# Optimization experiments

Hardware: AMD Instinct MI355X
Metric: run time of the kernel (lower is better)

## Reference

```python
import jax, jax.numpy as jnp
import numpy as np

BN_EPS = 1e-6
SOFTMAX_EPS = 1e-8
D = 64      # fingerprint_dim
BD = 12     # bond_dim
N_ATOM = 10000
N_EDGE = 40000


def _bn(x, gamma, beta, mean, var):
    # BatchNorm1d in inference mode (running stats)
    return (x - mean) / jnp.sqrt(var + BN_EPS) * gamma + beta


def setup_inputs() -> dict:
    key = jax.random.key(0)
    ks = jax.random.split(key, 16)
    inp = {
        "atom": jax.random.normal(ks[0], (N_ATOM, D), dtype=jnp.float32),
        "bond_index": jax.random.randint(ks[1], (N_EDGE, 2), 0, N_ATOM, dtype=jnp.int64),
        "bond": jax.random.normal(ks[2], (N_EDGE, BD), dtype=jnp.float32),
        # encoder: Linear(bond_dim, D*D) + BatchNorm1d(D*D)
        "enc_W": jax.random.normal(ks[3], (D * D, BD), dtype=jnp.float32) * (1.0 / np.sqrt(BD)),
        "enc_b": jnp.zeros((D * D,), dtype=jnp.float32),
        "enc_gamma": jnp.ones((D * D,), dtype=jnp.float32),
        "enc_beta": jnp.zeros((D * D,), dtype=jnp.float32),
        "enc_mean": jnp.zeros((D * D,), dtype=jnp.float32),
        "enc_var": jnp.ones((D * D,), dtype=jnp.float32),
        # align: Linear(2*D, 1)
        "align_W": jax.random.normal(ks[4], (1, 2 * D), dtype=jnp.float32) * (1.0 / np.sqrt(2 * D)),
        "align_b": jnp.zeros((1,), dtype=jnp.float32),
        # attend: Linear(D, D) + BatchNorm1d(D), no activation
        "att_W": jax.random.normal(ks[5], (D, D), dtype=jnp.float32) * (1.0 / np.sqrt(D)),
        "att_b": jnp.zeros((D,), dtype=jnp.float32),
        "att_gamma": jnp.ones((D,), dtype=jnp.float32),
        "att_beta": jnp.zeros((D,), dtype=jnp.float32),
        "att_mean": jnp.zeros((D,), dtype=jnp.float32),
        "att_var": jnp.ones((D,), dtype=jnp.float32),
        # GRUCell(D, D)
        "gru_W_ih": jax.random.normal(ks[6], (3 * D, D), dtype=jnp.float32) * (1.0 / np.sqrt(D)),
        "gru_W_hh": jax.random.normal(ks[7], (3 * D, D), dtype=jnp.float32) * (1.0 / np.sqrt(D)),
        "gru_b_ih": jnp.zeros((3 * D,), dtype=jnp.float32),
        "gru_b_hh": jnp.zeros((3 * D,), dtype=jnp.float32),
    }
    return inp


def reference(atom, bond_index, bond,
              enc_W, enc_b, enc_gamma, enc_beta, enc_mean, enc_var,
              align_W, align_b,
              att_W, att_b, att_gamma, att_beta, att_mean, att_var,
              gru_W_ih, gru_W_hh, gru_b_ih, gru_b_hh):
    num_atom, d = atom.shape
    tgt = bond_index[:, 0]  # target atom of each edge
    nbr = bond_index[:, 1]  # neighbor atom of each edge

    # encoder: relu(BN(linear(bond))) -> per-edge [d, d] bond matrix
    enc = jax.nn.relu(_bn(bond @ enc_W.T + enc_b, enc_gamma, enc_beta, enc_mean, enc_var))
    enc = enc.reshape(-1, d, d)  # [E, d, d]

    # gather neighbor atoms, per-edge matvec through bond matrix
    neighbor = jnp.einsum('ed,edf->ef', atom[nbr], enc)  # [E, d]

    # attention logits (dropout is identity in eval)
    feat = jnp.concatenate([atom[tgt], neighbor], axis=-1)  # [E, 2d]
    score = jax.nn.leaky_relu(feat @ align_W.T + align_b, negative_slope=0.01)  # [E, 1]

    # segment softmax over target atoms
    mx = jax.ops.segment_max(score, tgt, num_segments=num_atom)  # [N, 1]
    ex = jnp.exp(score - mx[tgt])
    denom = jax.ops.segment_sum(ex, tgt, num_segments=num_atom)[tgt] + SOFTMAX_EPS
    attn = ex / denom  # [E, 1]

    # attend: BN(linear(neighbor)) (no activation), weighted scatter-add
    attd = _bn(neighbor @ att_W.T + att_b, att_gamma, att_beta, att_mean, att_var)
    context = jax.ops.segment_sum(attn * attd, tgt, num_segments=num_atom)  # [N, d]
    context = jax.nn.elu(context)

    # GRUCell(context, atom)
    gi = context @ gru_W_ih.T + gru_b_ih  # [N, 3d]
    gh = atom @ gru_W_hh.T + gru_b_hh     # [N, 3d]
    i_r, i_z, i_n = jnp.split(gi, 3, axis=-1)
    h_r, h_z, h_n = jnp.split(gh, 3, axis=-1)
    r = jax.nn.sigmoid(i_r + h_r)
    z = jax.nn.sigmoid(i_z + h_z)
    n = jnp.tanh(i_n + r * h_n)
    return (1.0 - z) * n + z * atom
```

## Files before the change

### kernel.cpp

```cpp
#include <hip/hip_runtime.h>
#include <math.h>

#define NA 10000
#define NE 40000

typedef float f4 __attribute__((ext_vector_type(4)));
typedef float f16v __attribute__((ext_vector_type(16)));
typedef int   i4 __attribute__((ext_vector_type(4)));
typedef __bf16 bf16x8 __attribute__((ext_vector_type(8)));

union U8 { unsigned short us[8]; bf16x8 v; };

static __device__ __forceinline__ unsigned short bf_rne(float x){
  unsigned u = __float_as_uint(x);
  unsigned r = (u + 0x7fffu + ((u>>16)&1u)) >> 16;
  return (unsigned short)r;
}
static __device__ __forceinline__ float bf_to_f(unsigned short h){
  return __uint_as_float(((unsigned)h)<<16);
}

__global__ __launch_bounds__(256) void k_pre(
  const float* __restrict__ encW, const float* __restrict__ encB,
  const float* __restrict__ eg, const float* __restrict__ ebt,
  const float* __restrict__ e_mn, const float* __restrict__ e_vr,
  const float* __restrict__ attW, const float* __restrict__ attB,
  const float* __restrict__ agm, const float* __restrict__ abt,
  const float* __restrict__ amn, const float* __restrict__ avr,
  const float* __restrict__ wih, const float* __restrict__ whh,
  const int* __restrict__ bidx, const float* __restrict__ atom,
  const float* __restrict__ alW,
  unsigned short* __restrict__ Bh, unsigned short* __restrict__ Bl,
  unsigned short* __restrict__ aBh, unsigned short* __restrict__ aBl,
  float* __restrict__ attBf, float* __restrict__ wT,
  float* __restrict__ p, int* __restrict__ cnt)
{
  int tid = threadIdx.x;
  int gid = blockIdx.x*256 + tid;
  int gstride = gridDim.x*256;
  for (int i=gid; i<65536; i+=gstride){
    int j = i&7, ll = (i>>3)&63, t = i>>9;
    int d = t>>1, ft = t&1;
    int k = ((ll>>5)<<3)+j;
    int n = d*64 + ft*32 + (ll&31);
    float s = eg[n]*rsqrtf(e_vr[n]+1e-6f);
    unsigned short vh=0, vl=0;
    if (k<12){
      float wv = encW[n*12+k]*s;
      unsigned short hi = bf_rne(wv);
      vh = hi; vl = bf_rne(wv - bf_to_f(hi));
    } else if (k==12){
      float b = (encB[n]-e_mn[n])*s + ebt[n];
      unsigned short hi = bf_rne(b);
      vh = hi; vl = bf_rne(b - bf_to_f(hi));
    }
    Bh[i] = vh; Bl[i] = vl;
  }
  for (int i=gid; i<4096; i+=gstride){
    int j=i&7, l=(i>>3)&63, t=i>>9;
    int kk=t>>1, nt=t&1;
    int k = kk*16 + ((l>>5)<<3) + j;
    int n = nt*32 + (l&31);
    float s = agm[n]*rsqrtf(avr[n]+1e-6f);
    float wv = attW[n*64+k]*s;
    unsigned short hi = bf_rne(wv);
    aBh[i]=hi; aBl[i]=bf_rne(wv - bf_to_f(hi));
  }
  for (int f=gid; f<64; f+=gstride){
    float s = agm[f]*rsqrtf(avr[f]+1e-6f);
    attBf[f] = (attB[f]-amn[f])*s + abt[f];
  }
  for (int i=gid; i<24576; i+=gstride){
    int j=i&3, f=(i>>2)&63, idx2=i>>8;
    int g=idx2>>4, kg=idx2&15, k=kg*4+j;
    wT[i] = (g<3)? wih[(g*64+f)*64+k] : whh[((g-3)*64+f)*64+k];
  }
  {
    int wid = gid>>6;
    int l = tid&63;
    float wl = alW[l];
    for (int a=wid; a<NA; a+=(gstride>>6)){
      float v = wl*atom[(size_t)a*64+l];
      v += __shfl_xor(v,1);  v += __shfl_xor(v,2);
      v += __shfl_xor(v,4);  v += __shfl_xor(v,8);
      v += __shfl_xor(v,16); v += __shfl_xor(v,32);
      if (l==0) p[a]=v;
    }
  }
  for (int e=gid; e<NE; e+=gstride) atomicAdd(&cnt[bidx[e*2]],1);
}

__global__ __launch_bounds__(256) void k_scan(const int* __restrict__ cnt,
                                              int* __restrict__ rowstart,
                                              int* __restrict__ wofs)
{
  __shared__ int sPart[256];
  int t = threadIdx.x;
  int base = t*40;
  i4 buf[10];
  int sum = 0;
  if (base < NA){
    const i4* cp = (const i4*)(cnt + base);
    #pragma unroll
    for (int i=0;i<10;i++) buf[i] = cp[i];
    #pragma unroll
    for (int i=0;i<10;i++) sum += buf[i].x+buf[i].y+buf[i].z+buf[i].w;
  }
  sPart[t]=sum;
  __syncthreads();
  for (int off=1; off<256; off<<=1){
    int v = (t>=off)? sPart[t-off] : 0;
    __syncthreads();
    sPart[t]+=v;
    __syncthreads();
  }
  int run = sPart[t]-sum;
  if (base < NA){
    #pragma unroll
    for (int i=0;i<10;i++){
      i4 b=buf[i], o;
      o.x=run; run+=b.x; o.y=run; run+=b.y;
      o.z=run; run+=b.z; o.w=run; run+=b.w;
      ((i4*)(rowstart+base))[i]=o;
      ((i4*)(wofs+base))[i]=o;
    }
  }
  if (t==0) rowstart[NA]=NE;
}

__global__ __launch_bounds__(256) void k_scatter(const int* __restrict__ bidx,
                                                 int* __restrict__ wofs,
                                                 int* __restrict__ elist)
{
  int e = blockIdx.x*256 + threadIdx.x;
  if (e < NE){
    int tg = bidx[e*2];
    int pos = atomicAdd(&wofs[tg],1);
    elist[pos]=e;
  }
}

__global__ __launch_bounds__(256) void k_edge(
  const float* __restrict__ atom, const int* __restrict__ bidx, const float* __restrict__ bond,
  const unsigned short* __restrict__ Bh, const unsigned short* __restrict__ Bl,
  const int* __restrict__ elist, float* __restrict__ nbC)
{
  __shared__ float sA[2304];
  __shared__ float sP[4096];
  __shared__ int   sEl[32];
  __shared__ int   sNbr[32];

  int tid = threadIdx.x;
  int l = tid & 63;
  int w = tid >> 6;
  int g = l >> 5;
  int em = l & 31;
  int E0 = blockIdx.x * 32;

  if (tid < 32){
    int e = elist[E0+tid];
    sEl[tid] = e;
    sNbr[tid] = bidx[e*2+1];
  }
  __syncthreads();
  for (int i=tid; i<2048; i+=256){
    int le=i>>6, d=i&63;
    sA[d*36+le] = atom[(size_t)sNbr[le]*64 + d];
  }

  U8 A1, A2;
  {
    const f4* bp = (const f4*)(bond + (size_t)sEl[em]*12);
    f4 b0=bp[0], b1v=bp[1], b2v=bp[2];
    float bv[12] = {b0.x,b0.y,b0.z,b0.w,b1v.x,b1v.y,b1v.z,b1v.w,b2v.x,b2v.y,b2v.z,b2v.w};
    unsigned short hi[12], lo2[12];
    #pragma unroll
    for (int j=0;j<12;j++){ hi[j]=bf_rne(bv[j]); lo2[j]=bf_rne(bv[j]-bf_to_f(hi[j])); }
    #pragma unroll
    for (int j=0;j<8;j++){
      int k = g*8+j;
      A1.us[j] = (k<12)? hi[k] : (k==12? (unsigned short)0x3F80 : (unsigned short)0);
      A2.us[j] = (k<12)? lo2[k] : (unsigned short)0;
    }
  }
  __syncthreads();

  int ft = w & 1;
  int dbase = (w >> 1) * 32;

  f4 nacc[4];
  #pragma unroll
  for (int q=0;q<4;q++) nacc[q] = (f4){0.f,0.f,0.f,0.f};
  f16v cz;
  #pragma unroll
  for (int r=0;r<16;r++) cz[r] = 0.f;

  U8 cbh, cbl;
  cbh.v = *(const bf16x8*)(Bh + ((size_t)((dbase*2+ft)*64 + l))*8);
  cbl.v = *(const bf16x8*)(Bl + ((size_t)((dbase*2+ft)*64 + l))*8);

  #pragma unroll 2
  for (int dd=0; dd<32; dd++){
    int d = dbase + dd;
    int dn = (dd<31)? d+1 : d;
    U8 nbh, nbl;
    nbh.v = *(const bf16x8*)(Bh + ((size_t)((dn*2+ft)*64 + l))*8);
    nbl.v = *(const bf16x8*)(Bl + ((size_t)((dn*2+ft)*64 + l))*8);

    f4 ldA[4];
    #pragma unroll
    for (int q=0;q<4;q++) ldA[q] = *(const f4*)&sA[d*36 + 8*q + 4*g];

    f16v c;
    c = __builtin_amdgcn_mfma_f32_32x32x16_bf16(A1.v, cbh.v, cz, 0,0,0);
    c = __builtin_amdgcn_mfma_f32_32x32x16_bf16(A2.v, cbh.v, c, 0,0,0);
    c = __builtin_amdgcn_mfma_f32_32x32x16_bf16(A1.v, cbl.v, c, 0,0,0);
    #pragma unroll
    for (int r=0;r<16;r++){
      float ev = fmaxf(c[r], 0.f);
      nacc[r>>2][r&3] = fmaf(ldA[r>>2][r&3], ev, nacc[r>>2][r&3]);
    }
    cbh = nbh; cbl = nbl;
  }

  #pragma unroll
  for (int r=0;r<16;r++)
    sP[w*1024 + r*64 + l] = nacc[r>>2][r&3];
  __syncthreads();

  if (w < 2){
    #pragma unroll 4
    for (int r=0;r<16;r++){
      int idx = r*64 + l;
      float v = sP[w*1024 + idx] + sP[(w+2)*1024 + idx];
      int m = (r&3) + ((r>>2)<<3) + ((l>>5)<<2);
      int f = (w<<5) + (l&31);
      nbC[(size_t)(E0+m)*64 + f] = v;
    }
  }
}

__global__ __launch_bounds__(256) void k_zq(
  const float* __restrict__ nbC,
  const unsigned short* __restrict__ aBh, const unsigned short* __restrict__ aBl,
  const float* __restrict__ alW,
  float* __restrict__ zC, float* __restrict__ qv)
{
  __shared__ float sNb[64*68];
  int tid = threadIdx.x;
  int l = tid & 63;
  int w = tid >> 6;
  int g = l >> 5;
  int em = l & 31;
  int E0 = blockIdx.x * 64;

  for (int i=tid; i<4096; i+=256){
    int le=i>>6, f=i&63;
    sNb[le*68+f] = nbC[(size_t)(E0+le)*64 + f];
  }
  __syncthreads();

  {
    float alwn = alW[64+l];
    #pragma unroll 4
    for (int i=0;i<16;i++){
      int le = w*16 + i;
      float qq = sNb[le*68 + l] * alwn;
      qq += __shfl_xor(qq,1);  qq += __shfl_xor(qq,2);
      qq += __shfl_xor(qq,4);  qq += __shfl_xor(qq,8);
      qq += __shfl_xor(qq,16); qq += __shfl_xor(qq,32);
      if (l==0) qv[E0+le] = qq;
    }
  }

  {
    f16v c;
    #pragma unroll
    for (int r=0;r<16;r++) c[r] = 0.f;
    int mt2 = w>>1, nt = w&1;
    #pragma unroll
    for (int kk=0; kk<4; kk++){
      const float* src = &sNb[(mt2*32+em)*68 + kk*16 + g*8];
      f4 x0 = *(const f4*)src;
      f4 x1 = *(const f4*)(src+4);
      U8 Ah, Al;
      #pragma unroll
      for (int j=0;j<4;j++){
        unsigned short h0 = bf_rne(x0[j]);
        Ah.us[j] = h0; Al.us[j] = bf_rne(x0[j]-bf_to_f(h0));
        unsigned short h1 = bf_rne(x1[j]);
        Ah.us[4+j] = h1; Al.us[4+j] = bf_rne(x1[j]-bf_to_f(h1));
      }
      U8 bh, bl;
      bh.v = *(const bf16x8*)(aBh + ((size_t)((kk*2+nt)*64 + l))*8);
      bl.v = *(const bf16x8*)(aBl + ((size_t)((kk*2+nt)*64 + l))*8);
      c = __builtin_amdgcn_mfma_f32_32x32x16_bf16(Ah.v, bh.v, c, 0,0,0);
      c = __builtin_amdgcn_mfma_f32_32x32x16_bf16(Al.v, bh.v, c, 0,0,0);
      c = __builtin_amdgcn_mfma_f32_32x32x16_bf16(Ah.v, bl.v, c, 0,0,0);
    }
    #pragma unroll
    for (int r=0;r<16;r++){
      int row = (r&3) + ((r>>2)<<3) + ((l>>5)<<2);
      zC[(size_t)(E0 + mt2*32 + row)*64 + nt*32 + (l&31)] = c[r];
    }
  }
}

__global__ __launch_bounds__(256, 4) void k_gru(
  const float* __restrict__ atom, const float* __restrict__ zC,
  const int* __restrict__ rowstart, const float* __restrict__ p,
  const float* __restrict__ qv, const float* __restrict__ alB,
  const float* __restrict__ attBf, const float* __restrict__ wT,
  const float* __restrict__ bih, const float* __restrict__ bhh,
  float* __restrict__ out)
{
  __shared__ float sc[4][2][64];
  __shared__ float shh[4][2][64];
  int tid = threadIdx.x;
  int l = tid & 63;
  int w = tid >> 6;
  int base = blockIdx.x*8 + w*2;
  float bias = attBf[l];
  float ab = alB[0];

  #pragma unroll
  for (int aa=0; aa<2; aa++){
    int a = base + aa;
    float cf=0.f, hf=0.f;
    if (a < NA){
      hf = atom[(size_t)a*64 + l];
      int d0 = rowstart[a];
      int deg = rowstart[a+1] - d0;
      if (deg > 0){
        float pa = p[a] + ab;
        float mx = -1e30f;
        #pragma unroll 1
        for (int i=0;i<deg;i++){
          float s = pa + qv[d0+i];
          s = (s>0.f)? s : 0.01f*s;
          mx = fmaxf(mx, s);
        }
        float dn = 0.f, y = 0.f;
        #pragma unroll 1
        for (int i=0;i<deg;i++){
          float s = pa + qv[d0+i];
          s = (s>0.f)? s : 0.01f*s;
          float ex = __expf(s - mx);
          dn += ex;
          y = fmaf(ex, zC[(size_t)(d0+i)*64 + l], y);
        }
        cf = (y + dn*bias)/(dn + 1e-8f);
        cf = (cf>0.f)? cf : expm1f(cf);
      }
    }
    sc[w][aa][l] = cf; shh[w][aa][l] = hf;
  }
  __syncthreads();

  float acc[6][2];
  #pragma unroll
  for (int gg=0;gg<6;gg++){ acc[gg][0]=0.f; acc[gg][1]=0.f; }

  #pragma unroll 2
  for (int kg=0; kg<16; kg++){
    f4 wv[6];
    #pragma unroll
    for (int gg=0;gg<6;gg++) wv[gg] = *(const f4*)&wT[(size_t)((gg*16+kg)*64 + l)*4];
    #pragma unroll
    for (int aa=0;aa<2;aa++){
      f4 cv = *(const f4*)&sc[w][aa][kg*4];
      f4 hv = *(const f4*)&shh[w][aa][kg*4];
      #pragma unroll
      for (int j=0;j<4;j++){
        acc[0][aa] = fmaf(cv[j], wv[0][j], acc[0][aa]);
        acc[1][aa] = fmaf(cv[j], wv[1][j], acc[1][aa]);
        acc[2][aa] = fmaf(cv[j], wv[2][j], acc[2][aa]);
        acc[3][aa] = fmaf(hv[j], wv[3][j], acc[3][aa]);
        acc[4][aa] = fmaf(hv[j], wv[4][j], acc[4][aa]);
        acc[5][aa] = fmaf(hv[j], wv[5][j], acc[5][aa]);
      }
    }
  }

  float b0 = bih[l], b1 = bih[64+l], b2 = bih[128+l];
  float h0 = bhh[l], h1 = bhh[64+l], h2 = bhh[128+l];
  #pragma unroll
  for (int aa=0;aa<2;aa++){
    int a = base + aa;
    if (a < NA){
      float hf = shh[w][aa][l];
      float r = 1.f/(1.f + expf(-(acc[0][aa] + b0 + acc[3][aa] + h0)));
      float z = 1.f/(1.f + expf(-(acc[1][aa] + b1 + acc[4][aa] + h1)));
      float n = tanhf(acc[2][aa] + b2 + r*(acc[5][aa] + h2));
      out[(size_t)a*64 + l] = (1.f - z)*n + z*hf;
    }
  }
}

extern "C" void kernel_launch(void* const* d_in, const int* in_sizes, int n_in,
                              void* d_out, int out_size, void* d_ws, size_t ws_size,
                              hipStream_t stream) {
  const float* atom = (const float*)d_in[0];
  const int*   bidx = (const int*)  d_in[1];
  const float* bond = (const float*)d_in[2];
  const float* encW = (const float*)d_in[3];
  const float* encB = (const float*)d_in[4];
  const float* eg   = (const float*)d_in[5];
  const float* ebt  = (const float*)d_in[6];
  const float* e_mn = (const float*)d_in[7];
  const float* e_vr = (const float*)d_in[8];
  const float* alW  = (const float*)d_in[9];
  const float* alB  = (const float*)d_in[10];
  const float* atW  = (const float*)d_in[11];
  const float* atB  = (const float*)d_in[12];
  const float* agm  = (const float*)d_in[13];
  const float* abt  = (const float*)d_in[14];
  const float* amn  = (const float*)d_in[15];
  const float* avr  = (const float*)d_in[16];
  const float* wih  = (const float*)d_in[17];
  const float* whh  = (const float*)d_in[18];
  const float* bih  = (const float*)d_in[19];
  const float* bhh  = (const float*)d_in[20];

  float* ws = (float*)d_ws;
  unsigned short* Bh  = (unsigned short*)(ws + 0);
  unsigned short* Bl  = (unsigned short*)(ws + 32768);
  unsigned short* aBh = (unsigned short*)(ws + 65536);
  unsigned short* aBl = (unsigned short*)(ws + 67584);
  float* attBf   = ws + 69632;
  float* wT      = ws + 69696;
  float* p       = ws + 94272;
  int*   cnt     = (int*)(ws + 104288);
  int*   rowstart= (int*)(ws + 114304);
  int*   wofs    = (int*)(ws + 124320);
  int*   elist   = (int*)(ws + 134336);
  float* qv      = ws + 174336;
  float* nbC     = ws + 214336;
  float* outp    = (float*)d_out;

  hipMemsetAsync(cnt, 0, NA*sizeof(int), stream);
  k_pre<<<512, 256, 0, stream>>>(encW,encB,eg,ebt,e_mn,e_vr,
                                 atW,atB,agm,abt,amn,avr,
                                 wih,whh,bidx,atom,alW,
                                 Bh,Bl,aBh,aBl,attBf,wT,p,cnt);
  k_scan<<<1, 256, 0, stream>>>(cnt, rowstart, wofs);
  k_scatter<<<(NE+255)/256, 256, 0, stream>>>(bidx, wofs, elist);
  k_edge<<<1250, 256, 0, stream>>>(atom, bidx, bond, Bh, Bl, elist, nbC);
  k_zq<<<625, 256, 0, stream>>>(nbC, aBh, aBl, alW, nbC , qv);
  k_gru<<<1250, 256, 0, stream>>>(atom, nbC, rowstart, p, qv, alB,
                                  attBf, wT, bih, bhh, outp);
}
```

Before: 187.3 us.

## Fuse edge neighbor computation with attention projection kernel, 64 edges per block

Merges k_edge and k_zq into one kernel. Each block now handles 64 edges instead of 32, and the per-edge neighbor vectors stay in shared memory (reusing sA) instead of going out to global memory and being read back. This removes one kernel launch and a full write plus read of the E×64 intermediate. It also reuses each loaded bond-matrix fragment across two MFMA tiles. In exchange, per-thread registers and shared memory grow and the grid halves to 625 blocks, which may lower occupancy and parallelism.

```diff
diff --git a/kernel.cpp b/kernel.cpp
--- a/kernel.cpp
+++ b/kernel.cpp
@@ -143,34 +143,37 @@
 __global__ __launch_bounds__(256) void k_edge(
   const float* __restrict__ atom, const int* __restrict__ bidx, const float* __restrict__ bond,
   const unsigned short* __restrict__ Bh, const unsigned short* __restrict__ Bl,
-  const int* __restrict__ elist, float* __restrict__ nbC)
+  const unsigned short* __restrict__ aBh, const unsigned short* __restrict__ aBl,
+  const float* __restrict__ alW,
+  const int* __restrict__ elist, float* __restrict__ zC, float* __restrict__ qv)
 {
-  __shared__ float sA[2304];
+  __shared__ float sA[4352];
   __shared__ float sP[4096];
-  __shared__ int   sEl[32];
-  __shared__ int   sNbr[32];
+  __shared__ int   sEl[64];
+  __shared__ int   sNbr[64];
 
   int tid = threadIdx.x;
   int l = tid & 63;
   int w = tid >> 6;
   int g = l >> 5;
   int em = l & 31;
-  int E0 = blockIdx.x * 32;
-
-  if (tid < 32){
+  int E0 = blockIdx.x * 64;
+
+  if (tid < 64){
     int e = elist[E0+tid];
     sEl[tid] = e;
     sNbr[tid] = bidx[e*2+1];
   }
   __syncthreads();
-  for (int i=tid; i<2048; i+=256){
+  for (int i=tid; i<4096; i+=256){
     int le=i>>6, d=i&63;
-    sA[d*36+le] = atom[(size_t)sNbr[le]*64 + d];
-  }
-
-  U8 A1, A2;
-  {
-    const f4* bp = (const f4*)(bond + (size_t)sEl[em]*12);
+    sA[d*68+le] = atom[(size_t)sNbr[le]*64 + d];
+  }
+
+  U8 A1[2], A2[2];
+  #pragma unroll
+  for (int t=0;t<2;t++){
+    const f4* bp = (const f4*)(bond + (size_t)sEl[t*32+em]*12);
     f4 b0=bp[0], b1v=bp[1], b2v=bp[2];
     float bv[12] = {b0.x,b0.y,b0.z,b0.w,b1v.x,b1v.y,b1v.z,b1v.w,b2v.x,b2v.y,b2v.z,b2v.w};
     unsigned short hi[12], lo2[12];
@@ -179,8 +182,8 @@
     #pragma unroll
     for (int j=0;j<8;j++){
       int k = g*8+j;
-      A1.us[j] = (k<12)? hi[k] : (k==12? (unsigned short)0x3F80 : (unsigned short)0);
-      A2.us[j] = (k<12)? lo2[k] : (unsigned short)0;
+      A1[t].us[j] = (k<12)? hi[k] : (k==12? (unsigned short)0x3F80 : (unsigned short)0);
+      A2[t].us[j] = (k<12)? lo2[k] : (unsigned short)0;
     }
   }
   __syncthreads();
@@ -188,9 +191,11 @@
   int ft = w & 1;
   int dbase = (w >> 1) * 32;
 
-  f4 nacc[4];
-  #pragma unroll
-  for (int q=0;q<4;q++) nacc[q] = (f4){0.f,0.f,0.f,0.f};
+  f4 nacc[2][4];
+  #pragma unroll
+  for (int t=0;t<2;t++)
+    #pragma unroll
+    for (int q=0;q<4;q++) nacc[t][q] = (f4){0.f,0.f,0.f,0.f};
   f16v cz;
   #pragma unroll
   for (int r=0;r<16;r++) cz[r] = 0.f;
@@ -207,56 +212,45 @@
     nbh.v = *(const bf16x8*)(Bh + ((size_t)((dn*2+ft)*64 + l))*8);
     nbl.v = *(const bf16x8*)(Bl + ((size_t)((dn*2+ft)*64 + l))*8);
 
-    f4 ldA[4];
-    #pragma unroll
-    for (int q=0;q<4;q++) ldA[q] = *(const f4*)&sA[d*36 + 8*q + 4*g];
-
-    f16v c;
-    c = __builtin_amdgcn_mfma_f32_32x32x16_bf16(A1.v, cbh.v, cz, 0,0,0);
-    c = __builtin_amdgcn_mfma_f32_32x32x16_bf16(A2.v, cbh.v, c, 0,0,0);
-    c = __builtin_amdgcn_mfma_f32_32x32x16_bf16(A1.v, cbl.v, c, 0,0,0);
-    #pragma unroll
-    for (int r=0;r<16;r++){
-      float ev = fmaxf(c[r], 0.f);
-      nacc[r>>2][r&3] = fmaf(ldA[r>>2][r&3], ev, nacc[r>>2][r&3]);
+    f4 ldA[2][4];
+    #pragma unroll
+    for (int t=0;t<2;t++)
+      #pragma unroll
+      for (int q=0;q<4;q++) ldA[t][q] = *(const f4*)&sA[d*68 + t*32 + 8*q + 4*g];
+
+    #pragma unroll
+    for (int t=0;t<2;t++){
+      f16v c;
+      c = __builtin_amdgcn_mfma_f32_32x32x16_bf16(A1[t].v, cbh.v, cz, 0,0,0);
+      c = __builtin_amdgcn_mfma_f32_32x32x16_bf16(A2[t].v, cbh.v, c, 0,0,0);
+      c = __builtin_amdgcn_mfma_f32_32x32x16_bf16(A1[t].v, cbl.v, c, 0,0,0);
+      #pragma unroll
+      for (int r=0;r<16;r++){
+        float ev = fmaxf(c[r], 0.f);
+        nacc[t][r>>2][r&3] = fmaf(ldA[t][r>>2][r&3], ev, nacc[t][r>>2][r&3]);
+      }
     }
     cbh = nbh; cbl = nbl;
   }
 
-  #pragma unroll
-  for (int r=0;r<16;r++)
-    sP[w*1024 + r*64 + l] = nacc[r>>2][r&3];
-  __syncthreads();
-
+  __syncthreads();
+  if (w >= 2){
+    #pragma unroll
+    for (int t=0;t<2;t++)
+      #pragma unroll
+      for (int r=0;r<16;r++)
+        sP[(w-2)*2048 + t*1024 + r*64 + l] = nacc[t][r>>2][r&3];
+  }
+  __syncthreads();
   if (w < 2){
-    #pragma unroll 4
-    for (int r=0;r<16;r++){
-      int idx = r*64 + l;
-      float v = sP[w*1024 + idx] + sP[(w+2)*1024 + idx];
-      int m = (r&3) + ((r>>2)<<3) + ((l>>5)<<2);
-      int f = (w<<5) + (l&31);
-      nbC[(size_t)(E0+m)*64 + f] = v;
-    }
-  }
-}
-
-__global__ __launch_bounds__(256) void k_zq(
-  const float* __restrict__ nbC,
-  const unsigned short* __restrict__ aBh, const unsigned short* __restrict__ aBl,
-  const float* __restrict__ alW,
-  float* __restrict__ zC, float* __restrict__ qv)
-{
-  __shared__ float sNb[64*68];
-  int tid = threadIdx.x;
-  int l = tid & 63;
-  int w = tid >> 6;
-  int g = l >> 5;
-  int em = l & 31;
-  int E0 = blockIdx.x * 64;
-
-  for (int i=tid; i<4096; i+=256){
-    int le=i>>6, f=i&63;
-    sNb[le*68+f] = nbC[(size_t)(E0+le)*64 + f];
+    #pragma unroll
+    for (int t=0;t<2;t++)
+      #pragma unroll
+      for (int r=0;r<16;r++){
+        float v = nacc[t][r>>2][r&3] + sP[w*2048 + t*1024 + r*64 + l];
+        int m = t*32 + (r&3) + ((r>>2)<<3) + (g<<2);
+        sA[m*68 + (w<<5) + em] = v;
+      }
   }
   __syncthreads();
 
@@ -265,14 +259,13 @@
     #pragma unroll 4
     for (int i=0;i<16;i++){
       int le = w*16 + i;
-      float qq = sNb[le*68 + l] * alwn;
+      float qq = sA[le*68 + l] * alwn;
       qq += __shfl_xor(qq,1);  qq += __shfl_xor(qq,2);
       qq += __shfl_xor(qq,4);  qq += __shfl_xor(qq,8);
       qq += __shfl_xor(qq,16); qq += __shfl_xor(qq,32);
       if (l==0) qv[E0+le] = qq;
     }
   }
-
   {
     f16v c;
     #pragma unroll
@@ -280,7 +273,7 @@
     int mt2 = w>>1, nt = w&1;
     #pragma unroll
     for (int kk=0; kk<4; kk++){
-      const float* src = &sNb[(mt2*32+em)*68 + kk*16 + g*8];
+      const float* src = &sA[(mt2*32+em)*68 + kk*16 + g*8];
       f4 x0 = *(const f4*)src;
       f4 x1 = *(const f4*)(src+4);
       U8 Ah, Al;
@@ -435,7 +428,7 @@
   int*   wofs    = (int*)(ws + 124320);
   int*   elist   = (int*)(ws + 134336);
   float* qv      = ws + 174336;
-  float* nbC     = ws + 214336;
+  float* zCb     = ws + 214336;
   float* outp    = (float*)d_out;
 
   hipMemsetAsync(cnt, 0, NA*sizeof(int), stream);
@@ -445,8 +438,8 @@
                                  Bh,Bl,aBh,aBl,attBf,wT,p,cnt);
   k_scan<<<1, 256, 0, stream>>>(cnt, rowstart, wofs);
   k_scatter<<<(NE+255)/256, 256, 0, stream>>>(bidx, wofs, elist);
-  k_edge<<<1250, 256, 0, stream>>>(atom, bidx, bond, Bh, Bl, elist, nbC);
-  k_zq<<<625, 256, 0, stream>>>(nbC, aBh, aBl, alW, nbC , qv);
-  k_gru<<<1250, 256, 0, stream>>>(atom, nbC, rowstart, p, qv, alB,
+  k_edge<<<625, 256, 0, stream>>>(atom, bidx, bond, Bh, Bl, aBh, aBl, alW,
+                                  elist, zCb, qv);
+  k_gru<<<1250, 256, 0, stream>>>(atom, zCb, rowstart, p, qv, alB,
                                   attBf, wT, bih, bhh, outp);
 }
```

Measured after the change: 183.1 us. 1.02x faster.
